# Kernel optimization log

Hardware: AMD Instinct MI355X
Metric: run time of the kernel (lower is better)

Reference implementation:

```python
import jax, jax.numpy as jnp
import numpy as np

DIM = 1024
NUM_HEADS = 16
HEAD_DIM = DIM // NUM_HEADS
BINDING_BIAS = 0.5
SCALE = HEAD_DIM ** -0.5


def setup_inputs() -> dict:
    key = jax.random.key(0)
    ks = jax.random.split(key, 10)
    B, S, D = 2, 2048, DIM
    std = D ** -0.5
    return {
        "x": jax.random.normal(ks[0], (B, S, D), jnp.float32),
        "binding_matrix": jax.random.uniform(ks[1], (S, S), jnp.float32),
        "Wq": jax.random.normal(ks[2], (D, D), jnp.float32) * std,
        "bq": jnp.zeros((D,), jnp.float32),
        "Wk": jax.random.normal(ks[3], (D, D), jnp.float32) * std,
        "bk": jnp.zeros((D,), jnp.float32),
        "Wv": jax.random.normal(ks[4], (D, D), jnp.float32) * std,
        "bv": jnp.zeros((D,), jnp.float32),
        "Wo": jax.random.normal(ks[5], (D, D), jnp.float32) * std,
        "bo": jnp.zeros((D,), jnp.float32),
    }


def reference(x, binding_matrix, Wq, bq, Wk, bk, Wv, bv, Wo, bo):
    B, S, D = x.shape
    H, Hd = NUM_HEADS, HEAD_DIM
    # projections -> [B, H, S, Hd]
    q = (x @ Wq + bq).reshape(B, S, H, Hd).transpose(0, 2, 1, 3)
    k = (x @ Wk + bk).reshape(B, S, H, Hd).transpose(0, 2, 1, 3)
    v = (x @ Wv + bv).reshape(B, S, H, Hd).transpose(0, 2, 1, 3)
    # scores [B, H, S, S] with additive binding bias
    attn = jnp.einsum("bhqd,bhkd->bhqk", q, k) * SCALE
    attn = attn + BINDING_BIAS * binding_matrix[None, None, :, :]
    attn = jax.nn.softmax(attn, axis=-1)
    out = jnp.einsum("bhqk,bhkd->bhqd", attn, v)
    out = out.transpose(0, 2, 1, 3).reshape(B, S, D)
    return out @ Wo + bo
```

## Files before the change

### kernel.cpp

```cpp
#include <hip/hip_runtime.h>

#define DEV static __device__ __forceinline__

typedef __attribute__((ext_vector_type(4))) float f32x4;
typedef __attribute__((ext_vector_type(8))) __bf16 bfv8;
typedef __attribute__((ext_vector_type(8))) short s8v;
typedef __attribute__((ext_vector_type(4))) short s4v;

DEV short f2bf(float f) {
    unsigned u = __float_as_uint(f);
    u = (u + 0x7fffu + ((u >> 16) & 1u)) >> 16;
    return (short)u;
}
DEV float bf2f(short s) { return __uint_as_float(((unsigned)(unsigned short)s) << 16); }

DEV void gload16(const void* g, void* l) {
    __builtin_amdgcn_global_load_lds(
        (const __attribute__((address_space(1))) void*)g,
        (__attribute__((address_space(3))) void*)l, 16, 0, 0);
}

DEV f32x4 mfma16(bfv8 a, bfv8 b, f32x4 c) {
    return __builtin_amdgcn_mfma_f32_16x16x32_bf16(a, b, c, 0, 0, 0);
}

DEV float max3f(float a, float b, float c) {
    float d;
    asm("v_max3_f32 %0, %1, %2, %3" : "=v"(d) : "v"(a), "v"(b), "v"(c));
    return d;
}
DEV unsigned cvtpk(float lo, float hi) {
    unsigned w;
    asm("v_cvt_pk_bf16_f32 %0, %1, %2" : "=v"(w) : "v"(lo), "v"(hi));
    return w;
}

DEV bfv8 ldsfrag(const short* base, int row, int slog) {
    int sp = slog ^ (row & 7);
    return *reinterpret_cast<const bfv8*>(base + row * 64 + sp * 8);
}

__global__ void k_cvt(const float* __restrict__ in, short* __restrict__ out, float s) {
    int i = blockIdx.x * blockDim.x + threadIdx.x;
    const float4* p = (const float4*)in + (size_t)i * 2;
    float4 a = p[0], b = p[1];
    s8v o;
    o[0] = f2bf(a.x * s); o[1] = f2bf(a.y * s); o[2] = f2bf(a.z * s); o[3] = f2bf(a.w * s);
    o[4] = f2bf(b.x * s); o[5] = f2bf(b.y * s); o[6] = f2bf(b.z * s); o[7] = f2bf(b.w * s);
    reinterpret_cast<s8v*>(out)[i] = o;
}

__global__ void k_cvtb(const float* __restrict__ in, short* __restrict__ out, float s) {
    int i = blockIdx.x * blockDim.x + threadIdx.x;
    int ktn = i >> 11, q = i & 2047;
    const float4* p = reinterpret_cast<const float4*>(in + (size_t)q * 2048 + ktn * 16);
    float4 a = p[0], b = p[1], cc = p[2], d = p[3];
    s8v o0, o1;
    o0[0] = f2bf(a.x * s); o0[1] = f2bf(a.y * s); o0[2] = f2bf(a.z * s); o0[3] = f2bf(a.w * s);
    o0[4] = f2bf(b.x * s); o0[5] = f2bf(b.y * s); o0[6] = f2bf(b.z * s); o0[7] = f2bf(b.w * s);
    o1[0] = f2bf(cc.x * s); o1[1] = f2bf(cc.y * s); o1[2] = f2bf(cc.z * s); o1[3] = f2bf(cc.w * s);
    o1[4] = f2bf(d.x * s); o1[5] = f2bf(d.y * s); o1[6] = f2bf(d.z * s); o1[7] = f2bf(d.w * s);
    s8v* dst = reinterpret_cast<s8v*>(out + (size_t)i * 16);
    dst[0] = o0; dst[1] = o1;
}

__global__ void k_transpose4(
    const float* __restrict__ W0, const float* __restrict__ W1,
    const float* __restrict__ W2, const float* __restrict__ W3,
    short* __restrict__ T0, short* __restrict__ T1,
    short* __restrict__ T2, short* __restrict__ T3, float s0)
{
    __shared__ float tl[32][33];
    const int z = blockIdx.z;
    const float* W = z == 0 ? W0 : z == 1 ? W1 : z == 2 ? W2 : W3;
    short* Wt = z == 0 ? T0 : z == 1 ? T1 : z == 2 ? T2 : T3;
    const float s = z == 0 ? s0 : 1.f;
    int tx = threadIdx.x & 31, ty = threadIdx.x >> 5;
    int nb = blockIdx.x * 32, kb = blockIdx.y * 32;
#pragma unroll
    for (int i = 0; i < 4; i++)
        tl[ty + i * 8][tx] = W[(kb + ty + i * 8) * 1024 + nb + tx];
    __syncthreads();
#pragma unroll
    for (int i = 0; i < 4; i++)
        Wt[(nb + ty + i * 8) * 1024 + kb + tx] = f2bf(tl[tx][ty + i * 8] * s);
}

template <int EPI>
DEV void gemm_body(const short* __restrict__ A, const short* __restrict__ Bt,
                   const float* __restrict__ bias, void* __restrict__ outp,
                   float bscale, int row0, int col0, short* As, short* Bs)
{
    const int t = threadIdx.x, lane = t & 63;
    const int wv = t >> 6, wr = wv >> 1, wc = wv & 1;
    const int g = lane >> 4, c = lane & 15;

    const f32x4 z4 = {0.f, 0.f, 0.f, 0.f};
    f32x4 acc[2][4];
#pragma unroll
    for (int m = 0; m < 2; m++)
#pragma unroll
        for (int n = 0; n < 4; n++) acc[m][n] = z4;

    for (int kt = 0; kt < 16; ++kt) {
        const int k0 = kt * 64;
        const short* Ag = A + row0 * 1024 + k0;
        const short* Bg = Bt + col0 * 1024 + k0;
#pragma unroll
        for (int j = 0; j < 2; j++) {
            int idx = j * 256 + t;
            int row = idx >> 3, sp = idx & 7, sl = sp ^ (row & 7);
            gload16(Ag + row * 1024 + sl * 8, As + idx * 8);
        }
#pragma unroll
        for (int j = 0; j < 4; j++) {
            int idx = j * 256 + t;
            int row = idx >> 3, sp = idx & 7, sl = sp ^ (row & 7);
            gload16(Bg + row * 1024 + sl * 8, Bs + idx * 8);
        }
        __syncthreads();

        bfv8 af[2][2], bfr[4][2];
#pragma unroll
        for (int m = 0; m < 2; m++)
#pragma unroll
            for (int ks = 0; ks < 2; ks++)
                af[m][ks] = ldsfrag(As, wr * 32 + m * 16 + c, ks * 4 + g);
#pragma unroll
        for (int n = 0; n < 4; n++)
#pragma unroll
            for (int ks = 0; ks < 2; ks++)
                bfr[n][ks] = ldsfrag(Bs, wc * 64 + n * 16 + c, ks * 4 + g);
        __builtin_amdgcn_s_setprio(1);
#pragma unroll
        for (int m = 0; m < 2; m++)
#pragma unroll
            for (int n = 0; n < 4; n++)
#pragma unroll
                for (int ks = 0; ks < 2; ks++)
                    acc[m][n] = mfma16(af[m][ks], bfr[n][ks], acc[m][n]);
        __builtin_amdgcn_s_setprio(0);
        __syncthreads();
    }

#pragma unroll
    for (int n = 0; n < 4; n++) {
        const int gc = col0 + wc * 64 + n * 16 + c;
        const float bvl = bias[gc] * bscale;
        const int h = gc >> 6, d = gc & 63;
#pragma unroll
        for (int m = 0; m < 2; m++) {
            const int gr = row0 + wr * 32 + m * 16 + g * 4;
            if (EPI == 2) {
                float* O = (float*)outp;
#pragma unroll
                for (int r = 0; r < 4; r++) O[(gr + r) * 1024 + gc] = acc[m][n][r] + bvl;
            } else {
                const int b = gr >> 11, sr = gr & 2047;
                short* O = (short*)outp;
                if (EPI == 0) {
                    int base = ((b * 16 + h) * 2048 + sr) * 64 + d;
#pragma unroll
                    for (int r = 0; r < 4; r++) O[base + r * 64] = f2bf(acc[m][n][r] + bvl);
                } else {
                    s4v vv;
#pragma unroll
                    for (int r = 0; r < 4; r++) vv[r] = f2bf(acc[m][n][r] + bvl);
                    const int s6 = sr & 63;
                    const int qp = (sr & ~63) | (s6 & 35) | ((s6 & 12) << 1) | ((s6 & 16) >> 2);
                    *reinterpret_cast<s4v*>(O + ((b * 16 + h) * 64 + d) * 2048 + qp) = vv;
                }
            }
        }
    }
}

__global__ __launch_bounds__(256, 2) void k_gemm3(
    const short* __restrict__ A,
    const short* __restrict__ WqT, const short* __restrict__ WkT, const short* __restrict__ WvT,
    const float* __restrict__ bq, const float* __restrict__ bk, const float* __restrict__ bv,
    short* __restrict__ Qs, short* __restrict__ Kst, short* __restrict__ Vts, float scq)
{
    __shared__ alignas(16) short As[64 * 64];
    __shared__ alignas(16) short Bs[128 * 64];
    const int which = blockIdx.y >> 3;
    const int col0 = (blockIdx.y & 7) * 128;
    const int row0 = blockIdx.x * 64;
    if (which == 0)
        gemm_body<0>(A, WqT, bq, Qs, scq, row0, col0, As, Bs);
    else if (which == 1)
        gemm_body<0>(A, WkT, bk, Kst, 1.f, row0, col0, As, Bs);
    else
        gemm_body<1>(A, WvT, bv, Vts, 1.f, row0, col0, As, Bs);
}

__global__ __launch_bounds__(256, 2) void k_gemmO(
    const short* __restrict__ A, const short* __restrict__ Bt,
    const float* __restrict__ bias, float* __restrict__ outp)
{
    __shared__ alignas(16) short As[64 * 64];
    __shared__ alignas(16) short Bs[128 * 64];
    gemm_body<2>(A, Bt, bias, outp, 1.f, blockIdx.x * 64, blockIdx.y * 128, As, Bs);
}

__global__ __launch_bounds__(512, 2) void k_attn(
    const short* __restrict__ Q, const short* __restrict__ K,
    const short* __restrict__ Vt, const short* __restrict__ bbt,
    short* __restrict__ Ob)
{
    __shared__ alignas(16) short Ks[2][64 * 64];
    __shared__ alignas(16) short Vs[2][64 * 64];
    const int t = threadIdx.x, lane = t & 63;
    const int wv = t >> 6, g = lane >> 4, c = lane & 15;
    const int qt = blockIdx.x, bh = blockIdx.y;
    const int b = bh >> 4, h = bh & 15;
    const short* Qb = Q + bh * 2048 * 64;
    const short* Kb = K + bh * 2048 * 64;
    const short* Vb = Vt + bh * 64 * 2048;
    const int q0 = qt * 128 + wv * 16;

    bfv8 qf[2];
#pragma unroll
    for (int ks = 0; ks < 2; ks++)
        qf[ks] = *reinterpret_cast<const bfv8*>(Qb + (q0 + c) * 64 + ks * 32 + g * 8);

    const f32x4 z4 = {0.f, 0.f, 0.f, 0.f};
    f32x4 oa[4];
#pragma unroll
    for (int nd = 0; nd < 4; nd++) oa[nd] = z4;
    f32x4 lacc = z4;
    float mrun = 20.0f;

    s8v ob_;
#pragma unroll
    for (int i = 0; i < 8; i++) ob_[i] = (short)0x3F80;
    const bfv8 ones = __builtin_bit_cast(bfv8, ob_);

    const int r0 = t >> 3, s0 = ((t & 7) ^ (r0 & 7)) * 8;
    const short* kp0 = Kb + r0 * 64 + s0;
    const short* vp0 = Vb + r0 * 2048 + s0;
    const int dst8 = t * 8;
    const short* bbp = bbt + (size_t)(q0 + c) * 16 + 4 * g;

    const int cx = c & 7;
    const int fofs0 = c * 128 + ((g ^ cx) << 4);
    const int fofs1 = c * 128 + (((4 + g) ^ cx) << 4);

    gload16(kp0, &Ks[0][dst8]);
    gload16(vp0, &Vs[0][dst8]);
    kp0 += 4096; vp0 += 64;
    s4v bn[4];
#pragma unroll
    for (int n = 0; n < 4; n++)
        bn[n] = *reinterpret_cast<const s4v*>(bbp + n * 32768);
    bbp += 131072;
    __syncthreads();

    for (int kt = 0; kt < 32; ++kt) {
        const int cur = kt & 1;
        f32x4 cb[4];
#pragma unroll
        for (int n = 0; n < 4; n++)
#pragma unroll
            for (int r = 0; r < 4; r++) cb[n][r] = bf2f(bn[n][r]);
        if (kt < 31) {
            const int nb = cur ^ 1;
            gload16(kp0, &Ks[nb][dst8]);
            gload16(vp0, &Vs[nb][dst8]);
            kp0 += 4096; vp0 += 64;
#pragma unroll
            for (int n = 0; n < 4; n++)
                bn[n] = *reinterpret_cast<const s4v*>(bbp + n * 32768);
            bbp += 131072;
        }

        const char* Kc = (const char*)&Ks[cur][0];
        const char* Vc = (const char*)&Vs[cur][0];

        f32x4 sc[4];
        __builtin_amdgcn_s_setprio(1);
#pragma unroll
        for (int n = 0; n < 4; n++) {
            bfv8 k0 = *reinterpret_cast<const bfv8*>(Kc + fofs0 + n * 2048);
            bfv8 k1 = *reinterpret_cast<const bfv8*>(Kc + fofs1 + n * 2048);
            sc[n] = mfma16(k0, qf[0], cb[n]);
            sc[n] = mfma16(k1, qf[1], sc[n]);
        }
        __builtin_amdgcn_s_setprio(0);

#pragma unroll
        for (int n = 0; n < 4; n++)
#pragma unroll
            for (int r = 0; r < 4; r++)
                sc[n][r] = __builtin_amdgcn_exp2f(sc[n][r] - mrun);

        unsigned w0[4], w1[4];
#pragma unroll
        for (int n = 0; n < 4; n++) {
            w0[n] = cvtpk(sc[n][0], sc[n][1]);
            w1[n] = cvtpk(sc[n][2], sc[n][3]);
        }
        typedef struct { unsigned a, b, c2, d; } u4;
        u4 q0w; q0w.a = w0[0]; q0w.b = w1[0]; q0w.c2 = w0[1]; q0w.d = w1[1];
        u4 q1w; q1w.a = w0[2]; q1w.b = w1[2]; q1w.c2 = w0[3]; q1w.d = w1[3];
        const bfv8 pf0 = __builtin_bit_cast(bfv8, q0w);
        const bfv8 pf1 = __builtin_bit_cast(bfv8, q1w);

        __builtin_amdgcn_s_setprio(1);
#pragma unroll
        for (int nd = 0; nd < 4; nd++) {
            bfv8 v0 = *reinterpret_cast<const bfv8*>(Vc + fofs0 + nd * 2048);
            bfv8 v1 = *reinterpret_cast<const bfv8*>(Vc + fofs1 + nd * 2048);
            oa[nd] = mfma16(v0, pf0, oa[nd]);
            oa[nd] = mfma16(v1, pf1, oa[nd]);
        }
        lacc = mfma16(ones, pf0, lacc);
        lacc = mfma16(ones, pf1, lacc);
        __builtin_amdgcn_s_setprio(0);

        float t0 = fmaxf(max3f(sc[0][0], sc[0][1], sc[0][2]), sc[0][3]);
        float t1 = fmaxf(max3f(sc[1][0], sc[1][1], sc[1][2]), sc[1][3]);
        float t2 = fmaxf(max3f(sc[2][0], sc[2][1], sc[2][2]), sc[2][3]);
        float t3 = fmaxf(max3f(sc[3][0], sc[3][1], sc[3][2]), sc[3][3]);
        float pemax = fmaxf(max3f(t0, t1, t2), t3);
        if (!__all(pemax <= 2896.0f)) {
            float rmax = fmaxf(pemax, __shfl_xor(pemax, 16));
            rmax = fmaxf(rmax, __shfl_xor(rmax, 32));
            if (rmax > 2896.0f) {
                const float corr = 1.0f / rmax;
                mrun += __log2f(rmax);
#pragma unroll
                for (int nd = 0; nd < 4; nd++)
#pragma unroll
                    for (int r = 0; r < 4; r++) oa[nd][r] *= corr;
#pragma unroll
                for (int r = 0; r < 4; r++) lacc[r] *= corr;
            }
        }
        __syncthreads();
    }

    const float rl = 1.0f / lacc[0];
    const size_t srow = (size_t)(b * 2048 + q0 + c);
#pragma unroll
    for (int nd = 0; nd < 4; nd++) {
        s4v st;
#pragma unroll
        for (int r = 0; r < 4; r++) st[r] = f2bf(oa[nd][r] * rl);
        *reinterpret_cast<s4v*>(Ob + srow * 1024 + h * 64 + nd * 16 + 4 * g) = st;
    }
}

extern "C" void kernel_launch(void* const* d_in, const int* in_sizes, int n_in,
                              void* d_out, int out_size, void* d_ws, size_t ws_size,
                              hipStream_t stream)
{
    (void)in_sizes; (void)n_in; (void)out_size; (void)ws_size;
    const float* x    = (const float*)d_in[0];
    const float* bind = (const float*)d_in[1];
    const float* Wq   = (const float*)d_in[2];
    const float* bq   = (const float*)d_in[3];
    const float* Wk   = (const float*)d_in[4];
    const float* bk   = (const float*)d_in[5];
    const float* Wv   = (const float*)d_in[6];
    const float* bv   = (const float*)d_in[7];
    const float* Wo   = (const float*)d_in[8];
    const float* bo   = (const float*)d_in[9];

    char* ws = (char*)d_ws;
    const size_t MB = (size_t)1 << 20;
    short* xb   = (short*)(ws + 0 * MB);
    short* Wqt  = (short*)(ws + 8 * MB);
    short* Wkt  = (short*)(ws + 10 * MB);
    short* Wvt  = (short*)(ws + 12 * MB);
    short* Wot  = (short*)(ws + 14 * MB);
    short* bbm  = (short*)(ws + 16 * MB);
    short* Qs   = (short*)(ws + 24 * MB);
    short* Kst  = (short*)(ws + 32 * MB);
    short* Vts  = (short*)(ws + 40 * MB);
    short* Obuf = (short*)(ws + 48 * MB);

    const float LOG2E = 1.4426950408889634f;
    const float SCQ = 0.125f * LOG2E;
    const float SCB = 0.5f * LOG2E;

    k_cvt<<<2048, 256, 0, stream>>>(x, xb, 1.f);
    k_cvtb<<<1024, 256, 0, stream>>>(bind, bbm, SCB);
    k_transpose4<<<dim3(32, 32, 4), 256, 0, stream>>>(Wq, Wk, Wv, Wo,
                                                      Wqt, Wkt, Wvt, Wot, SCQ);
    k_gemm3<<<dim3(64, 24), 256, 0, stream>>>(xb, Wqt, Wkt, Wvt, bq, bk, bv,
                                              Qs, Kst, Vts, SCQ);
    k_attn<<<dim3(16, 32), 512, 0, stream>>>(Qs, Kst, Vts, bbm, Obuf);
    k_gemmO<<<dim3(64, 8), 256, 0, stream>>>(Obuf, Wot, bo, (float*)d_out);
}
```

Measured before the change: 125.4 us.

## Enlarge QKV GEMM tile to 128x128 and attention block to 256 queries

The QKV projection GEMM now uses 128x128 output tiles (each wave holds a 4x4 MFMA accumulator grid), which halves the grid and raises operand reuse per LDS load. The attention kernel goes from 512 to 1024 threads per block, covering 256 queries, so each K/V tile loaded into LDS serves twice as many query rows. Its K and V loads are split so the first 512 threads fetch K and the rest fetch V. In exchange there is more register pressure, fewer blocks (256 attention blocks on the GPU), and possible occupancy limits from launch_bounds(1024,4).

```diff
diff --git a/kernel.cpp b/kernel.cpp
--- a/kernel.cpp
+++ b/kernel.cpp
@@ -87,6 +87,34 @@
 }
 
 template <int EPI>
+DEV void gemm_store(f32x4 a4, int gr, int gc, const float* bias, float bscale,
+                    void* outp)
+{
+    const float bvl = bias[gc] * bscale;
+    const int h = gc >> 6, d = gc & 63;
+    if (EPI == 2) {
+        float* O = (float*)outp;
+#pragma unroll
+        for (int r = 0; r < 4; r++) O[(gr + r) * 1024 + gc] = a4[r] + bvl;
+    } else {
+        const int b = gr >> 11, sr = gr & 2047;
+        short* O = (short*)outp;
+        if (EPI == 0) {
+            int base = ((b * 16 + h) * 2048 + sr) * 64 + d;
+#pragma unroll
+            for (int r = 0; r < 4; r++) O[base + r * 64] = f2bf(a4[r] + bvl);
+        } else {
+            s4v vv;
+#pragma unroll
+            for (int r = 0; r < 4; r++) vv[r] = f2bf(a4[r] + bvl);
+            const int s6 = sr & 63;
+            const int qp = (sr & ~63) | (s6 & 35) | ((s6 & 12) << 1) | ((s6 & 16) >> 2);
+            *reinterpret_cast<s4v*>(O + ((b * 16 + h) * 64 + d) * 2048 + qp) = vv;
+        }
+    }
+}
+
+template <int EPI>
 DEV void gemm_body(const short* __restrict__ A, const short* __restrict__ Bt,
                    const float* __restrict__ bias, void* __restrict__ outp,
                    float bscale, int row0, int col0, short* As, short* Bs)
@@ -146,32 +174,72 @@
 #pragma unroll
     for (int n = 0; n < 4; n++) {
         const int gc = col0 + wc * 64 + n * 16 + c;
-        const float bvl = bias[gc] * bscale;
-        const int h = gc >> 6, d = gc & 63;
-#pragma unroll
-        for (int m = 0; m < 2; m++) {
-            const int gr = row0 + wr * 32 + m * 16 + g * 4;
-            if (EPI == 2) {
-                float* O = (float*)outp;
-#pragma unroll
-                for (int r = 0; r < 4; r++) O[(gr + r) * 1024 + gc] = acc[m][n][r] + bvl;
-            } else {
-                const int b = gr >> 11, sr = gr & 2047;
-                short* O = (short*)outp;
-                if (EPI == 0) {
-                    int base = ((b * 16 + h) * 2048 + sr) * 64 + d;
-#pragma unroll
-                    for (int r = 0; r < 4; r++) O[base + r * 64] = f2bf(acc[m][n][r] + bvl);
-                } else {
-                    s4v vv;
-#pragma unroll
-                    for (int r = 0; r < 4; r++) vv[r] = f2bf(acc[m][n][r] + bvl);
-                    const int s6 = sr & 63;
-                    const int qp = (sr & ~63) | (s6 & 35) | ((s6 & 12) << 1) | ((s6 & 16) >> 2);
-                    *reinterpret_cast<s4v*>(O + ((b * 16 + h) * 64 + d) * 2048 + qp) = vv;
-                }
-            }
-        }
+#pragma unroll
+        for (int m = 0; m < 2; m++)
+            gemm_store<EPI>(acc[m][n], row0 + wr * 32 + m * 16 + g * 4, gc,
+                            bias, bscale, outp);
+    }
+}
+
+template <int EPI>
+DEV void gemm_body128(const short* __restrict__ A, const short* __restrict__ Bt,
+                      const float* __restrict__ bias, void* __restrict__ outp,
+                      float bscale, int row0, int col0, short* As, short* Bs)
+{
+    const int t = threadIdx.x, lane = t & 63;
+    const int wv = t >> 6, wr = wv >> 1, wc = wv & 1;
+    const int g = lane >> 4, c = lane & 15;
+
+    const f32x4 z4 = {0.f, 0.f, 0.f, 0.f};
+    f32x4 acc[4][4];
+#pragma unroll
+    for (int m = 0; m < 4; m++)
+#pragma unroll
+        for (int n = 0; n < 4; n++) acc[m][n] = z4;
+
+    for (int kt = 0; kt < 16; ++kt) {
+        const int k0 = kt * 64;
+        const short* Ag = A + row0 * 1024 + k0;
+        const short* Bg = Bt + col0 * 1024 + k0;
+#pragma unroll
+        for (int j = 0; j < 4; j++) {
+            int idx = j * 256 + t;
+            int row = idx >> 3, sp = idx & 7, sl = sp ^ (row & 7);
+            gload16(Ag + row * 1024 + sl * 8, As + idx * 8);
+            gload16(Bg + row * 1024 + sl * 8, Bs + idx * 8);
+        }
+        __syncthreads();
+
+        bfv8 af[4][2], bfr[4][2];
+#pragma unroll
+        for (int m = 0; m < 4; m++)
+#pragma unroll
+            for (int ks = 0; ks < 2; ks++)
+                af[m][ks] = ldsfrag(As, wr * 64 + m * 16 + c, ks * 4 + g);
+#pragma unroll
+        for (int n = 0; n < 4; n++)
+#pragma unroll
+            for (int ks = 0; ks < 2; ks++)
+                bfr[n][ks] = ldsfrag(Bs, wc * 64 + n * 16 + c, ks * 4 + g);
+        __builtin_amdgcn_s_setprio(1);
+#pragma unroll
+        for (int m = 0; m < 4; m++)
+#pragma unroll
+            for (int n = 0; n < 4; n++)
+#pragma unroll
+                for (int ks = 0; ks < 2; ks++)
+                    acc[m][n] = mfma16(af[m][ks], bfr[n][ks], acc[m][n]);
+        __builtin_amdgcn_s_setprio(0);
+        __syncthreads();
+    }
+
+#pragma unroll
+    for (int n = 0; n < 4; n++) {
+        const int gc = col0 + wc * 64 + n * 16 + c;
+#pragma unroll
+        for (int m = 0; m < 4; m++)
+            gemm_store<EPI>(acc[m][n], row0 + wr * 64 + m * 16 + g * 4, gc,
+                            bias, bscale, outp);
     }
 }
 
@@ -181,17 +249,17 @@
     const float* __restrict__ bq, const float* __restrict__ bk, const float* __restrict__ bv,
     short* __restrict__ Qs, short* __restrict__ Kst, short* __restrict__ Vts, float scq)
 {
-    __shared__ alignas(16) short As[64 * 64];
+    __shared__ alignas(16) short As[128 * 64];
     __shared__ alignas(16) short Bs[128 * 64];
     const int which = blockIdx.y >> 3;
     const int col0 = (blockIdx.y & 7) * 128;
-    const int row0 = blockIdx.x * 64;
+    const int row0 = blockIdx.x * 128;
     if (which == 0)
-        gemm_body<0>(A, WqT, bq, Qs, scq, row0, col0, As, Bs);
+        gemm_body128<0>(A, WqT, bq, Qs, scq, row0, col0, As, Bs);
     else if (which == 1)
-        gemm_body<0>(A, WkT, bk, Kst, 1.f, row0, col0, As, Bs);
+        gemm_body128<0>(A, WkT, bk, Kst, 1.f, row0, col0, As, Bs);
     else
-        gemm_body<1>(A, WvT, bv, Vts, 1.f, row0, col0, As, Bs);
+        gemm_body128<1>(A, WvT, bv, Vts, 1.f, row0, col0, As, Bs);
 }
 
 __global__ __launch_bounds__(256, 2) void k_gemmO(
@@ -203,7 +271,7 @@
     gemm_body<2>(A, Bt, bias, outp, 1.f, blockIdx.x * 64, blockIdx.y * 128, As, Bs);
 }
 
-__global__ __launch_bounds__(512, 2) void k_attn(
+__global__ __launch_bounds__(1024, 4) void k_attn(
     const short* __restrict__ Q, const short* __restrict__ K,
     const short* __restrict__ Vt, const short* __restrict__ bbt,
     short* __restrict__ Ob)
@@ -217,7 +285,7 @@
     const short* Qb = Q + bh * 2048 * 64;
     const short* Kb = K + bh * 2048 * 64;
     const short* Vb = Vt + bh * 64 * 2048;
-    const int q0 = qt * 128 + wv * 16;
+    const int q0 = qt * 256 + wv * 16;
 
     bfv8 qf[2];
 #pragma unroll
@@ -236,19 +304,20 @@
     for (int i = 0; i < 8; i++) ob_[i] = (short)0x3F80;
     const bfv8 ones = __builtin_bit_cast(bfv8, ob_);
 
-    const int r0 = t >> 3, s0 = ((t & 7) ^ (r0 & 7)) * 8;
-    const short* kp0 = Kb + r0 * 64 + s0;
-    const short* vp0 = Vb + r0 * 2048 + s0;
-    const int dst8 = t * 8;
+    const bool isK = t < 512;
+    const int sidx = isK ? t : t - 512;
+    const int srow = sidx >> 3, ssl = ((sidx & 7) ^ (srow & 7)) * 8;
+    const short* sp_ = isK ? (Kb + srow * 64 + ssl) : (Vb + srow * 2048 + ssl);
+    const int sinc = isK ? 4096 : 64;
+    const int dst8 = sidx * 8;
     const short* bbp = bbt + (size_t)(q0 + c) * 16 + 4 * g;
 
     const int cx = c & 7;
     const int fofs0 = c * 128 + ((g ^ cx) << 4);
     const int fofs1 = c * 128 + (((4 + g) ^ cx) << 4);
 
-    gload16(kp0, &Ks[0][dst8]);
-    gload16(vp0, &Vs[0][dst8]);
-    kp0 += 4096; vp0 += 64;
+    gload16(sp_, isK ? &Ks[0][dst8] : &Vs[0][dst8]);
+    sp_ += sinc;
     s4v bn[4];
 #pragma unroll
     for (int n = 0; n < 4; n++)
@@ -265,9 +334,8 @@
             for (int r = 0; r < 4; r++) cb[n][r] = bf2f(bn[n][r]);
         if (kt < 31) {
             const int nb = cur ^ 1;
-            gload16(kp0, &Ks[nb][dst8]);
-            gload16(vp0, &Vs[nb][dst8]);
-            kp0 += 4096; vp0 += 64;
+            gload16(sp_, isK ? &Ks[nb][dst8] : &Vs[nb][dst8]);
+            sp_ += sinc;
 #pragma unroll
             for (int n = 0; n < 4; n++)
                 bn[n] = *reinterpret_cast<const s4v*>(bbp + n * 32768);
@@ -341,13 +409,13 @@
     }
 
     const float rl = 1.0f / lacc[0];
-    const size_t srow = (size_t)(b * 2048 + q0 + c);
+    const size_t orow = (size_t)(b * 2048 + q0 + c);
 #pragma unroll
     for (int nd = 0; nd < 4; nd++) {
         s4v st;
 #pragma unroll
         for (int r = 0; r < 4; r++) st[r] = f2bf(oa[nd][r] * rl);
-        *reinterpret_cast<s4v*>(Ob + srow * 1024 + h * 64 + nd * 16 + 4 * g) = st;
+        *reinterpret_cast<s4v*>(Ob + orow * 1024 + h * 64 + nd * 16 + 4 * g) = st;
     }
 }
 
@@ -388,8 +456,8 @@
     k_cvtb<<<1024, 256, 0, stream>>>(bind, bbm, SCB);
     k_transpose4<<<dim3(32, 32, 4), 256, 0, stream>>>(Wq, Wk, Wv, Wo,
                                                       Wqt, Wkt, Wvt, Wot, SCQ);
-    k_gemm3<<<dim3(64, 24), 256, 0, stream>>>(xb, Wqt, Wkt, Wvt, bq, bk, bv,
+    k_gemm3<<<dim3(32, 24), 256, 0, stream>>>(xb, Wqt, Wkt, Wvt, bq, bk, bv,
                                               Qs, Kst, Vts, SCQ);
-    k_attn<<<dim3(16, 32), 512, 0, stream>>>(Qs, Kst, Vts, bbm, Obuf);
+    k_attn<<<dim3(8, 32), 1024, 0, stream>>>(Qs, Kst, Vts, bbm, Obuf);
     k_gemmO<<<dim3(64, 8), 256, 0, stream>>>(Obuf, Wot, bo, (float*)d_out);
 }
```

Measured after the change: 122.0 us (median of 3 runs). 1.03x faster.
